# Kernel tuning notes

Measured on AMD Instinct MI355X. Metric: run time of the kernel, lower is better.

## Reference

```python
import jax, jax.numpy as jnp
import numpy as np
import math

B, T, C = 2, 2048, 768
NH, HD = 12, 64  # n_head, head_dim

def setup_inputs() -> dict:
    key = jax.random.key(0)
    k1, k2, k3 = jax.random.split(key, 3)
    x = jax.random.normal(k1, (B, T, C), dtype=jnp.float32)
    mask = jnp.tril(jnp.ones((T, T), dtype=bool))[None, None]  # [1,1,T,T] causal
    Wqkv = jax.random.normal(k2, (C, 3 * C), dtype=jnp.float32) * (1.0 / math.sqrt(C))
    Wproj = jax.random.normal(k3, (C, C), dtype=jnp.float32) * (1.0 / math.sqrt(C))
    return {"x": x, "mask": mask, "Wqkv": Wqkv, "Wproj": Wproj}

def reference(x, mask, Wqkv, Wproj):
    b, t, c = x.shape
    qkv = x @ Wqkv  # [b,t,3c]
    q, k, v = jnp.split(qkv, 3, axis=-1)
    q = q.reshape(b, t, NH, HD).transpose(0, 2, 1, 3)  # [b,h,t,d]
    k = k.reshape(b, t, NH, HD).transpose(0, 2, 1, 3)
    v = v.reshape(b, t, NH, HD).transpose(0, 2, 1, 3)
    att = jnp.einsum('bhqd,bhkd->bhqk', q, k) / math.sqrt(HD)
    att = jnp.where(mask, att, -jnp.inf)
    att = jax.nn.softmax(att, axis=-1)
    out = jnp.einsum('bhqk,bhkd->bhqd', att, v)
    out = out.transpose(0, 2, 1, 3).reshape(b, t, c)
    return out @ Wproj
```

## Files before the change

kernel.cpp:

```cpp
#include <hip/hip_runtime.h>
#include <hip/hip_bf16.h>

#define T_   2048
#define C_   768
#define NH_  12
#define HD_  64
#define M_   (2*T_)
#define N1_  (3*C_)
#define PB_  ((size_t)NH_*T_*HD_)
#define KS_  0.180336880f
#define MK_  8.65617024f

typedef __attribute__((ext_vector_type(8))) short  short8;
typedef __attribute__((ext_vector_type(4))) short  shortx4;
typedef __attribute__((ext_vector_type(4))) float  floatx4;

__device__ __forceinline__ floatx4 mfma_bf16(short8 a, short8 b, floatx4 c) {
    return __builtin_amdgcn_mfma_f32_16x16x32_bf16(a, b, c, 0, 0, 0);
}
__device__ __forceinline__ float fast_exp2(float x) {
    return __builtin_amdgcn_exp2f(x);
}
__device__ __forceinline__ void lds_fence() {
    asm volatile("s_waitcnt lgkmcnt(0)" ::: "memory");
    __builtin_amdgcn_sched_barrier(0);
}
__device__ __forceinline__ void async_load16(const __hip_bfloat16* g, __hip_bfloat16* l) {
    __builtin_amdgcn_global_load_lds(
        (const __attribute__((address_space(1))) void*)g,
        (__attribute__((address_space(3))) void*)l, 16, 0, 0);
}

__global__ __launch_bounds__(256) void prep_all(const float* __restrict__ x,
                                                const float* __restrict__ wqkv,
                                                const float* __restrict__ wproj,
                                                __hip_bfloat16* __restrict__ xb,
                                                __hip_bfloat16* __restrict__ wqkvT,
                                                __hip_bfloat16* __restrict__ wprojT) {
    if (blockIdx.x < 3072) {
        const int idx = blockIdx.x * 256 + threadIdx.x;
        const floatx4 v = ((const floatx4*)x)[idx];
        union { __hip_bfloat16 h[4]; shortx4 s; } u;
#pragma unroll
        for (int j = 0; j < 4; j++) u.h[j] = __float2bfloat16(v[j]);
        ((shortx4*)xb)[idx] = u.s;
    } else if (blockIdx.x < 3936) {
        const int j  = (blockIdx.x - 3072) * 256 + threadIdx.x;
        const int k8 = j / N1_;
        const int n  = j - k8 * N1_;
        union { __hip_bfloat16 h[8]; short8 s; } u;
#pragma unroll
        for (int jj = 0; jj < 8; jj++)
            u.h[jj] = __float2bfloat16(wqkv[(size_t)(k8 * 8 + jj) * N1_ + n]);
        *(short8*)(wqkvT + (size_t)n * C_ + k8 * 8) = u.s;
    } else {
        const int j  = (blockIdx.x - 3936) * 256 + threadIdx.x;
        const int k8 = j / C_;
        const int n  = j - k8 * C_;
        union { __hip_bfloat16 h[8]; short8 s; } u;
#pragma unroll
        for (int jj = 0; jj < 8; jj++)
            u.h[jj] = __float2bfloat16(wproj[(size_t)(k8 * 8 + jj) * C_ + n]);
        *(short8*)(wprojT + (size_t)n * C_ + k8 * 8) = u.s;
    }
}

__global__ __launch_bounds__(256) void prep1(const float* __restrict__ x,
                                             const float* __restrict__ wqkv,
                                             __hip_bfloat16* __restrict__ xb,
                                             __hip_bfloat16* __restrict__ wqkvT) {
    if (blockIdx.x < 3072) {
        const int idx = blockIdx.x * 256 + threadIdx.x;
        const floatx4 v = ((const floatx4*)x)[idx];
        union { __hip_bfloat16 h[4]; shortx4 s; } u;
#pragma unroll
        for (int j = 0; j < 4; j++) u.h[j] = __float2bfloat16(v[j]);
        ((shortx4*)xb)[idx] = u.s;
    } else {
        const int j  = (blockIdx.x - 3072) * 256 + threadIdx.x;
        const int k8 = j / N1_;
        const int n  = j - k8 * N1_;
        union { __hip_bfloat16 h[8]; short8 s; } u;
#pragma unroll
        for (int jj = 0; jj < 8; jj++)
            u.h[jj] = __float2bfloat16(wqkv[(size_t)(k8 * 8 + jj) * N1_ + n]);
        *(short8*)(wqkvT + (size_t)n * C_ + k8 * 8) = u.s;
    }
}
__global__ __launch_bounds__(256) void prep2(const float* __restrict__ wproj,
                                             __hip_bfloat16* __restrict__ wprojT) {
    const int j  = blockIdx.x * 256 + threadIdx.x;
    const int k8 = j / C_;
    const int n  = j - k8 * C_;
    union { __hip_bfloat16 h[8]; short8 s; } u;
#pragma unroll
    for (int jj = 0; jj < 8; jj++)
        u.h[jj] = __float2bfloat16(wproj[(size_t)(k8 * 8 + jj) * C_ + n]);
    *(short8*)(wprojT + (size_t)n * C_ + k8 * 8) = u.s;
}

__global__ __launch_bounds__(256) void gemm_bt64x128(const __hip_bfloat16* __restrict__ A,
                                                     const __hip_bfloat16* __restrict__ Bt,
                                                     int N, int K,
                                                     __hip_bfloat16* __restrict__ O0,
                                                     __hip_bfloat16* __restrict__ O1,
                                                     __hip_bfloat16* __restrict__ O2) {
    __shared__ __align__(16) __hip_bfloat16 As[64 * 32];
    __shared__ __align__(16) __hip_bfloat16 Bs[128 * 32];

    const int tid  = threadIdx.x;
    const int n0   = blockIdx.x * 128;
    const int m0   = blockIdx.y * 64;
    const int wave = tid >> 6;
    const int ln   = tid & 63;
    const int l16  = ln & 15;
    const int q4   = ln >> 4;
    const int wm   = (wave >> 1) * 32;
    const int wn   = (wave & 1) * 64;

    const int lrow = ln >> 2;
    const int loct = (ln & 3) * 8;
    const __hip_bfloat16* ApD  = A  + (size_t)(m0 + wave * 16 + lrow) * K + loct;
    const __hip_bfloat16* BpD0 = Bt + (size_t)(n0 + (2 * wave)     * 16 + lrow) * K + loct;
    const __hip_bfloat16* BpD1 = Bt + (size_t)(n0 + (2 * wave + 1) * 16 + lrow) * K + loct;
    __hip_bfloat16* AsD  = As + wave * 512;
    __hip_bfloat16* BsD0 = Bs + (2 * wave) * 512;
    __hip_bfloat16* BsD1 = Bs + (2 * wave + 1) * 512;

    floatx4 acc[2][4];
#pragma unroll
    for (int i = 0; i < 2; i++)
#pragma unroll
        for (int j = 0; j < 4; j++) acc[i][j] = (floatx4){0.f, 0.f, 0.f, 0.f};

    for (int k0 = 0; k0 < K; k0 += 32) {
        __syncthreads();
        async_load16(ApD  + k0, AsD);
        async_load16(BpD0 + k0, BsD0);
        async_load16(BpD1 + k0, BsD1);
        __syncthreads();
        short8 af[2], bfr[4];
#pragma unroll
        for (int i = 0; i < 2; i++)
            af[i] = *(const short8*)(As + (wm + i * 16 + l16) * 32 + q4 * 8);
#pragma unroll
        for (int j = 0; j < 4; j++)
            bfr[j] = *(const short8*)(Bs + (wn + j * 16 + l16) * 32 + q4 * 8);
#pragma unroll
        for (int i = 0; i < 2; i++)
#pragma unroll
            for (int j = 0; j < 4; j++)
                acc[i][j] = mfma_bf16(af[i], bfr[j], acc[i][j]);
    }

#pragma unroll
    for (int i = 0; i < 2; i++) {
        const int mbase = m0 + wm + i * 16 + q4 * 4;
#pragma unroll
        for (int j = 0; j < 4; j++) {
            const int n = n0 + wn + j * 16 + l16;
            const int which = n / C_;
            const int rem   = n - which * C_;
            const int h     = rem >> 6;
            const int d     = rem & 63;
#pragma unroll
            for (int r = 0; r < 4; r++) {
                const int mm = mbase + r;
                const __hip_bfloat16 hv = __float2bfloat16(acc[i][j][r]);
                const int bh = (mm >> 11) * NH_ + h;
                const int t  = mm & (T_ - 1);
                if (which == 0)      O0[((size_t)bh * T_ + t) * HD_ + d] = hv;
                else if (which == 1) O1[((size_t)bh * T_ + t) * HD_ + d] = hv;
                else                 O2[((size_t)bh * HD_ + d) * T_ + t] = hv;
            }
        }
    }
}

__global__ __launch_bounds__(256) void gemm_bt64(const __hip_bfloat16* __restrict__ A,
                                                 const __hip_bfloat16* __restrict__ Bt,
                                                 int N, int K,
                                                 float* __restrict__ O0) {
    __shared__ __align__(16) __hip_bfloat16 As[64 * 40];
    __shared__ __align__(16) __hip_bfloat16 Bs[64 * 40];

    const int tid  = threadIdx.x;
    const int n0   = blockIdx.x * 64;
    const int m0   = blockIdx.y * 64;
    const int srow = tid >> 2;
    const int scol = (tid & 3) * 8;
    const int wave = tid >> 6;
    const int ln   = tid & 63;
    const int l16  = ln & 15;
    const int q4   = ln >> 4;
    const int wm   = (wave >> 1) * 32;
    const int wn   = (wave & 1) * 32;

    floatx4 acc[2][2];
#pragma unroll
    for (int i = 0; i < 2; i++)
#pragma unroll
        for (int j = 0; j < 2; j++) acc[i][j] = (floatx4){0.f, 0.f, 0.f, 0.f};

    const __hip_bfloat16* Ap = A  + (size_t)(m0 + srow) * K + scol;
    const __hip_bfloat16* Bp = Bt + (size_t)(n0 + srow) * K + scol;

    for (int k0 = 0; k0 < K; k0 += 32) {
        short8 av = *(const short8*)(Ap + k0);
        short8 bv = *(const short8*)(Bp + k0);
        __syncthreads();
        *(short8*)(As + srow * 40 + scol) = av;
        *(short8*)(Bs + srow * 40 + scol) = bv;
        __syncthreads();
        short8 af[2], bfr[2];
#pragma unroll
        for (int i = 0; i < 2; i++) {
            af[i]  = *(const short8*)(As + (wm + i * 16 + l16) * 40 + q4 * 8);
            bfr[i] = *(const short8*)(Bs + (wn + i * 16 + l16) * 40 + q4 * 8);
        }
#pragma unroll
        for (int i = 0; i < 2; i++)
#pragma unroll
            for (int j = 0; j < 2; j++)
                acc[i][j] = mfma_bf16(af[i], bfr[j], acc[i][j]);
    }

#pragma unroll
    for (int i = 0; i < 2; i++) {
        const int mbase = m0 + wm + i * 16 + q4 * 4;
#pragma unroll
        for (int j = 0; j < 2; j++) {
            const int n = n0 + wn + j * 16 + l16;
#pragma unroll
            for (int r = 0; r < 4; r++)
                O0[(size_t)(mbase + r) * N + n] = acc[i][j][r];
        }
    }
}

__global__ __launch_bounds__(256) void attn_fused(const __hip_bfloat16* __restrict__ Q,
                                                  const __hip_bfloat16* __restrict__ Kd,
                                                  const __hip_bfloat16* __restrict__ Vt,
                                                  __hip_bfloat16* __restrict__ O) {
    __shared__ __align__(16) __hip_bfloat16 plds[4][2][16][72];

    const int bh   = blockIdx.x;
    const int wid  = threadIdx.x >> 6;
    const int lane = threadIdx.x & 63;
    const int l16  = lane & 15;
    const int q4   = lane >> 4;
    const int i    = 63 - (int)blockIdx.y;
    const int q0A  = 32 * i;
    const int q0B  = 32 * i + 16;
    const int nch  = (i >> 1) + 1;

    const __hip_bfloat16* Qh = Q  + (size_t)bh * T_ * HD_;
    const __hip_bfloat16* Kh = Kd + (size_t)bh * T_ * HD_;
    const __hip_bfloat16* Vh = Vt + (size_t)bh * HD_ * T_;

    short8 aqA[2], aqB[2];
#pragma unroll
    for (int kt = 0; kt < 2; kt++) {
        aqA[kt] = *(const short8*)(Qh + (size_t)(q0A + l16) * HD_ + kt * 32 + q4 * 8);
        aqB[kt] = *(const short8*)(Qh + (size_t)(q0B + l16) * HD_ + kt * 32 + q4 * 8);
    }

    floatx4 accA[4], accB[4];
#pragma unroll
    for (int ct = 0; ct < 4; ct++) {
        accA[ct] = (floatx4){0.f, 0.f, 0.f, 0.f};
        accB[ct] = (floatx4){0.f, 0.f, 0.f, 0.f};
    }
    float sumA = 0.f, sumB = 0.f;

    for (int c = wid; c < nch; c += 4) {
        const int kv0 = c * 64;
        const bool diag = (c == nch - 1);

        short8 bk[4][2];
#pragma unroll
        for (int nt = 0; nt < 4; nt++)
#pragma unroll
            for (int kt = 0; kt < 2; kt++)
                bk[nt][kt] = *(const short8*)(Kh + (size_t)(kv0 + nt * 16 + l16) * HD_ + kt * 32 + q4 * 8);

        short8 bv[4][2];
#pragma unroll
        for (int ct = 0; ct < 4; ct++)
#pragma unroll
            for (int kt = 0; kt < 2; kt++)
                bv[ct][kt] = *(const short8*)(Vh + (size_t)(ct * 16 + l16) * T_ + kv0 + kt * 32 + q4 * 8);

        floatx4 sA[4], sB[4];
#pragma unroll
        for (int nt = 0; nt < 4; nt++) {
            sA[nt] = (floatx4){0.f, 0.f, 0.f, 0.f};
            sB[nt] = (floatx4){0.f, 0.f, 0.f, 0.f};
#pragma unroll
            for (int kt = 0; kt < 2; kt++) {
                sA[nt] = mfma_bf16(bk[nt][kt], aqA[kt], sA[nt]);
                sB[nt] = mfma_bf16(bk[nt][kt], aqB[kt], sB[nt]);
            }
        }

        if (diag) {
#pragma unroll
            for (int nt = 0; nt < 4; nt++) {
#pragma unroll
                for (int r = 0; r < 4; r++) {
                    const int kvg = kv0 + nt * 16 + q4 * 4 + r;
                    if (kvg > q0A + l16) sA[nt][r] = -3e38f;
                    if (kvg > q0B + l16) sB[nt][r] = -3e38f;
                }
            }
        }

#pragma unroll
        for (int nt = 0; nt < 4; nt++) {
            union { __hip_bfloat16 h[4]; shortx4 s; } uA, uB;
            float pA[4], pB[4];
#pragma unroll
            for (int r = 0; r < 4; r++) {
                pA[r] = fast_exp2(sA[nt][r] * KS_ - MK_);
                pB[r] = fast_exp2(sB[nt][r] * KS_ - MK_);
                uA.h[r] = __float2bfloat16(pA[r]);
                uB.h[r] = __float2bfloat16(pB[r]);
            }
            sumA += (pA[0] + pA[1]) + (pA[2] + pA[3]);
            sumB += (pB[0] + pB[1]) + (pB[2] + pB[3]);
            *(shortx4*)(&plds[wid][0][l16][nt * 16 + q4 * 4]) = uA.s;
            *(shortx4*)(&plds[wid][1][l16][nt * 16 + q4 * 4]) = uB.s;
        }

        lds_fence();

        short8 apA[2], apB[2];
#pragma unroll
        for (int kt = 0; kt < 2; kt++) {
            apA[kt] = *(const short8*)(&plds[wid][0][l16][kt * 32 + q4 * 8]);
            apB[kt] = *(const short8*)(&plds[wid][1][l16][kt * 32 + q4 * 8]);
        }
#pragma unroll
        for (int ct = 0; ct < 4; ct++)
#pragma unroll
            for (int kt = 0; kt < 2; kt++) {
                accA[ct] = mfma_bf16(apA[kt], bv[ct][kt], accA[ct]);
                accB[ct] = mfma_bf16(apB[kt], bv[ct][kt], accB[ct]);
            }

        lds_fence();
    }

    sumA += __shfl_xor(sumA, 16, 64);
    sumA += __shfl_xor(sumA, 32, 64);
    sumB += __shfl_xor(sumB, 16, 64);
    sumB += __shfl_xor(sumB, 32, 64);

    __syncthreads();
    floatx4* accbuf = (floatx4*)&plds[0][0][0][0];
    float*   lbuf   = (float*)((char*)&plds[0][0][0][0] + 16384);

    auto publish = [&](int slot) {
#pragma unroll
        for (int ct = 0; ct < 4; ct++) {
            accbuf[((slot * 2 + 0) * 4 + ct) * 64 + lane] = accA[ct];
            accbuf[((slot * 2 + 1) * 4 + ct) * 64 + lane] = accB[ct];
        }
        if (q4 == 0) {
            lbuf[(slot * 2 + 0) * 16 + l16] = sumA;
            lbuf[(slot * 2 + 1) * 16 + l16] = sumB;
        }
    };
    auto mergeIn = [&](int slot) {
#pragma unroll
        for (int ct = 0; ct < 4; ct++) {
            accA[ct] += accbuf[((slot * 2 + 0) * 4 + ct) * 64 + lane];
            accB[ct] += accbuf[((slot * 2 + 1) * 4 + ct) * 64 + lane];
        }
        sumA += lbuf[(slot * 2 + 0) * 16 + l16];
        sumB += lbuf[(slot * 2 + 1) * 16 + l16];
    };

    if (wid >= 2) publish(wid - 2);
    __syncthreads();
    if (wid < 2) mergeIn(wid);
    __syncthreads();
    if (wid == 1) publish(0);
    __syncthreads();
    if (wid == 0) {
        mergeIn(0);
        const int orow0 = (bh / NH_) * T_;
        const int hcol  = (bh % NH_) * HD_;
#pragma unroll
        for (int r = 0; r < 4; r++) {
            const float invA = 1.0f / __shfl(sumA, q4 * 4 + r, 64);
            const float invB = 1.0f / __shfl(sumB, q4 * 4 + r, 64);
            __hip_bfloat16* oA = O + (size_t)(orow0 + q0A + q4 * 4 + r) * C_ + hcol;
            __hip_bfloat16* oB = O + (size_t)(orow0 + q0B + q4 * 4 + r) * C_ + hcol;
#pragma unroll
            for (int ct = 0; ct < 4; ct++) {
                oA[ct * 16 + l16] = __float2bfloat16(accA[ct][r] * invA);
                oB[ct * 16 + l16] = __float2bfloat16(accB[ct][r] * invB);
            }
        }
    }
}

extern "C" void kernel_launch(void* const* d_in, const int* in_sizes, int n_in,
                              void* d_out, int out_size, void* d_ws, size_t ws_size,
                              hipStream_t stream) {
    const float *x = nullptr, *wqkv = nullptr, *wproj = nullptr;
    for (int i = 0; i < n_in; i++) {
        const int s = in_sizes[i];
        if (s == M_ * C_ && !x) x = (const float*)d_in[i];
        else if (s == C_ * N1_ && !wqkv) wqkv = (const float*)d_in[i];
        else if (s == C_ * C_ && !wproj) wproj = (const float*)d_in[i];
    }
    float* out = (float*)d_out;
    __hip_bfloat16* ws = (__hip_bfloat16*)d_ws;
    __hip_bfloat16* Vt = (__hip_bfloat16*)d_out;

    __hip_bfloat16* Qall  = ws;
    __hip_bfloat16* Kall  = Qall + 2 * PB_;
    __hip_bfloat16* ATT   = Kall + 2 * PB_;
    __hip_bfloat16* xb    = ATT;
    __hip_bfloat16* wqkvT = (__hip_bfloat16*)d_out + 2 * PB_;

    const size_t needMerged = (6 * PB_ + (size_t)C_ * C_) * sizeof(__hip_bfloat16);
    if (ws_size >= needMerged) {
        __hip_bfloat16* wprojT = ws + 6 * PB_;
        prep_all<<<dim3(4224), 256, 0, stream>>>(x, wqkv, wproj, xb, wqkvT, wprojT);
        gemm_bt64x128<<<dim3(N1_ / 128, M_ / 64), 256, 0, stream>>>(
            xb, wqkvT, N1_, C_, Qall, Kall, Vt);
        attn_fused<<<dim3(2 * NH_, 64), 256, 0, stream>>>(Qall, Kall, Vt, ATT);
        gemm_bt64<<<dim3(C_ / 64, M_ / 64), 256, 0, stream>>>(ATT, wprojT, C_, C_, out);
    } else {
        __hip_bfloat16* wprojT = Qall;
        prep1<<<dim3(3936), 256, 0, stream>>>(x, wqkv, xb, wqkvT);
        gemm_bt64x128<<<dim3(N1_ / 128, M_ / 64), 256, 0, stream>>>(
            xb, wqkvT, N1_, C_, Qall, Kall, Vt);
        attn_fused<<<dim3(2 * NH_, 64), 256, 0, stream>>>(Qall, Kall, Vt, ATT);
        prep2<<<dim3(288), 256, 0, stream>>>(wproj, wprojT);
        gemm_bt64<<<dim3(C_ / 64, M_ / 64), 256, 0, stream>>>(ATT, wprojT, C_, C_, out);
    }
}
```

Baseline: 192.8 us.

## Double-buffer LDS tiles in QKV GEMM to overlap loads with MFMA

The QKV projection GEMM now uses two LDS buffers for the A and B tiles. It issues the async global-to-LDS loads for the next K-slice before running the MFMAs on the current slice, with one barrier per iteration instead of two. The aim is to hide global memory latency behind compute and cut barrier stalls. The cost is doubled LDS use for this kernel, which could reduce occupancy. Correctness relies on the barrier also waiting for the outstanding async loads.

```diff
diff --git a/kernel.cpp b/kernel.cpp
--- a/kernel.cpp
+++ b/kernel.cpp
@@ -105,8 +105,8 @@
                                                      __hip_bfloat16* __restrict__ O0,
                                                      __hip_bfloat16* __restrict__ O1,
                                                      __hip_bfloat16* __restrict__ O2) {
-    __shared__ __align__(16) __hip_bfloat16 As[64 * 32];
-    __shared__ __align__(16) __hip_bfloat16 Bs[128 * 32];
+    __shared__ __align__(16) __hip_bfloat16 As[2 * 64 * 32];
+    __shared__ __align__(16) __hip_bfloat16 Bs[2 * 128 * 32];
 
     const int tid  = threadIdx.x;
     const int n0   = blockIdx.x * 128;
@@ -123,9 +123,6 @@
     const __hip_bfloat16* ApD  = A  + (size_t)(m0 + wave * 16 + lrow) * K + loct;
     const __hip_bfloat16* BpD0 = Bt + (size_t)(n0 + (2 * wave)     * 16 + lrow) * K + loct;
     const __hip_bfloat16* BpD1 = Bt + (size_t)(n0 + (2 * wave + 1) * 16 + lrow) * K + loct;
-    __hip_bfloat16* AsD  = As + wave * 512;
-    __hip_bfloat16* BsD0 = Bs + (2 * wave) * 512;
-    __hip_bfloat16* BsD1 = Bs + (2 * wave + 1) * 512;
 
     floatx4 acc[2][4];
 #pragma unroll
@@ -133,24 +130,37 @@
 #pragma unroll
         for (int j = 0; j < 4; j++) acc[i][j] = (floatx4){0.f, 0.f, 0.f, 0.f};
 
-    for (int k0 = 0; k0 < K; k0 += 32) {
-        __syncthreads();
-        async_load16(ApD  + k0, AsD);
-        async_load16(BpD0 + k0, BsD0);
-        async_load16(BpD1 + k0, BsD1);
-        __syncthreads();
+    async_load16(ApD,  As + wave * 512);
+    async_load16(BpD0, Bs + (2 * wave) * 512);
+    async_load16(BpD1, Bs + (2 * wave + 1) * 512);
+    __syncthreads();
+
+    const int NT = K >> 5;
+    int cur = 0;
+    for (int t = 0; t < NT; ++t) {
+        if (t < NT - 1) {
+            const int k1 = (t + 1) * 32;
+            const int alt = (cur ^ 1);
+            async_load16(ApD  + k1, As + alt * 2048 + wave * 512);
+            async_load16(BpD0 + k1, Bs + alt * 4096 + (2 * wave) * 512);
+            async_load16(BpD1 + k1, Bs + alt * 4096 + (2 * wave + 1) * 512);
+        }
+        const __hip_bfloat16* Asc = As + cur * 2048;
+        const __hip_bfloat16* Bsc = Bs + cur * 4096;
         short8 af[2], bfr[4];
 #pragma unroll
         for (int i = 0; i < 2; i++)
-            af[i] = *(const short8*)(As + (wm + i * 16 + l16) * 32 + q4 * 8);
+            af[i] = *(const short8*)(Asc + (wm + i * 16 + l16) * 32 + q4 * 8);
 #pragma unroll
         for (int j = 0; j < 4; j++)
-            bfr[j] = *(const short8*)(Bs + (wn + j * 16 + l16) * 32 + q4 * 8);
+            bfr[j] = *(const short8*)(Bsc + (wn + j * 16 + l16) * 32 + q4 * 8);
 #pragma unroll
         for (int i = 0; i < 2; i++)
 #pragma unroll
             for (int j = 0; j < 4; j++)
                 acc[i][j] = mfma_bf16(af[i], bfr[j], acc[i][j]);
+        __syncthreads();
+        cur ^= 1;
     }
 
 #pragma unroll
```

Result: no change. 192.8 us (+0.0%).
